# Optimization experiments

Hardware: AMD Instinct MI355X
Metric: run time of the kernel (lower is better)

Reference implementation:

```python
import jax, jax.numpy as jnp
import numpy as np


def setup_inputs() -> dict:
    key = jax.random.key(0)
    k_x, k_w = jax.random.split(key)
    S, B, D, H = 2048, 16, 1024, 1024
    X = jax.random.normal(k_x, (S, B, D), dtype=jnp.float32)
    hidden = jnp.zeros((B, H), dtype=jnp.float32)  # initial C_0
    W = jax.random.normal(k_w, (3 * H, D), dtype=jnp.float32) * 0.02
    b = jnp.zeros((3 * H,), dtype=jnp.float32)
    return {"X": X, "hidden": hidden, "W": W, "b": b}


def reference(X, hidden, W, b):
    # QRNNLayer forward, window=1, output_gate=True, zoneout off (eval).
    # Linear projection: [S,B,D] @ [D,3H] -> [S,B,3H]
    Y = jnp.einsum('sbd,hd->sbh', X, W) + b
    Z, F, O = jnp.split(Y, 3, axis=2)
    Z = jnp.tanh(Z)
    F = jax.nn.sigmoid(F)
    O = jax.nn.sigmoid(O)

    # ForgetMult fo-pool: C_t = F_t * Z_t + (1 - F_t) * C_{t-1}
    def step(c, fz):
        f, z = fz
        c = f * z + (1.0 - f) * c
        return c, c

    _, C = jax.lax.scan(step, hidden, (F, Z))  # C: [S,B,H]
    H_out = O * C
    return H_out, C[-1:, :, :]  # (H, last cell state [1,B,H])
```

## Files before the change

### kernel.cpp

```cpp
#include <hip/hip_runtime.h>
#include <hip/hip_bf16.h>
#include <cstdint>
#include <cstddef>

#define S_LEN 2048
#define BATCH 16
#define DIM   1024
#define HID   1024
#define M_TOT (S_LEN * BATCH)
#define N_TOT (3 * HID)
#define K_TOT DIM
#define NCHUNK 32
#define CHLEN (S_LEN / NCHUNK)

#define BM 256
#define BN 256
#define BK 32
#define NT (K_TOT / BK)
#define GRID_M (M_TOT / BM)
#define GRID_N (N_TOT / BN)
#define NWG (GRID_M * GRID_N)

typedef __bf16 bf16x8 __attribute__((ext_vector_type(8)));
typedef float  f32x4  __attribute__((ext_vector_type(4)));

__device__ __forceinline__ unsigned short f2bf(float f) {
    unsigned int u = __float_as_uint(f);
    u += 0x7FFFu + ((u >> 16) & 1u);
    return (unsigned short)(u >> 16);
}
__device__ __forceinline__ float bf2f(unsigned int s) {
    return __uint_as_float(s << 16);
}
__device__ __forceinline__ float fast_sigmoid(float x) { return 1.0f / (1.0f + __expf(-x)); }
__device__ __forceinline__ float fast_tanh(float x)    { return 2.0f / (1.0f + __expf(-2.0f * x)) - 1.0f; }

__global__ void __launch_bounds__(256) cvt_f32_bf16(const float* __restrict__ in,
                                                    unsigned short* __restrict__ out, int n4) {
    int i = blockIdx.x * blockDim.x + threadIdx.x;
    const int stride = gridDim.x * blockDim.x;
    for (; i < n4; i += stride) {
        const float4 v = reinterpret_cast<const float4*>(in)[i];
        ushort4 o;
        o.x = f2bf(v.x); o.y = f2bf(v.y); o.z = f2bf(v.z); o.w = f2bf(v.w);
        reinterpret_cast<ushort4*>(out)[i] = o;
    }
}

#define GLOAD_LDS16(gp, lp)                                                         \
    __builtin_amdgcn_global_load_lds((__attribute__((address_space(1))) void*)(gp), \
                                     (__attribute__((address_space(3))) void*)(lp), 16, 0, 0)

__global__ void __launch_bounds__(512, 2)
gemm_gates(const unsigned short* __restrict__ Xb,
           const unsigned short* __restrict__ Wb,
           const float* __restrict__ bias,
           unsigned short* __restrict__ gates) {
    __shared__ unsigned short As[4][BM * BK];
    __shared__ unsigned short Bs[4][BN * BK];

    const int tid  = threadIdx.x;
    const int lane = tid & 63;
    const int wid  = tid >> 6;
    const int wm   = wid >> 2;
    const int wn   = wid & 3;
    const int lr   = lane & 15;
    const int lc   = lane >> 4;

    const int swz = (blockIdx.x & 7) * (NWG / 8) + (blockIdx.x >> 3);
    const int bn = swz % GRID_N;
    const int bm = swz / GRID_N;

    const int srow  = tid >> 2;
    const int scolE = (((tid & 3) ^ ((tid >> 3) & 3)) << 3);
    const unsigned short* gA = Xb + (size_t)(bm * BM + srow) * K_TOT + scolE;
    const unsigned short* gB = Wb + (size_t)(bn * BN + srow) * K_TOT + scolE;
    unsigned short* lA = &As[0][tid * 8];
    unsigned short* lB = &Bs[0][tid * 8];

#define STAGE(tt) do {                                                   \
        const int _s = (tt) & 3; const int _k = (tt) * BK;               \
        GLOAD_LDS16(gA + _k,                lA + _s * (BM * BK));        \
        GLOAD_LDS16(gA + 128 * K_TOT + _k,  lA + _s * (BM * BK) + 4096); \
        GLOAD_LDS16(gB + _k,                lB + _s * (BN * BK));        \
        GLOAD_LDS16(gB + 128 * K_TOT + _k,  lB + _s * (BN * BK) + 4096); \
    } while (0)

    f32x4 acc[8][4];
#pragma unroll
    for (int m = 0; m < 8; ++m)
#pragma unroll
        for (int n = 0; n < 4; ++n) acc[m][n] = {0.0f, 0.0f, 0.0f, 0.0f};

    STAGE(0); STAGE(1); STAGE(2);
    asm volatile("s_waitcnt vmcnt(8)" ::: "memory");
    __builtin_amdgcn_s_barrier();

    for (int t = 0; t < NT; ++t) {
        const int s = t & 3;
        bf16x8 av[8], bv[4];
#pragma unroll
        for (int m = 0; m < 8; ++m) {
            const int row = wm * 128 + m * 16 + lr;
            av[m] = *reinterpret_cast<const bf16x8*>(
                &As[s][row * BK + ((lc ^ ((row >> 1) & 3)) << 3)]);
        }
#pragma unroll
        for (int n = 0; n < 4; ++n) {
            const int row = wn * 64 + n * 16 + lr;
            bv[n] = *reinterpret_cast<const bf16x8*>(
                &Bs[s][row * BK + ((lc ^ ((row >> 1) & 3)) << 3)]);
        }
        if (t + 3 < NT) {
            STAGE(t + 3);
            asm volatile("s_waitcnt vmcnt(8)" ::: "memory");
        } else if (t + 3 == NT) {
            asm volatile("s_waitcnt vmcnt(4)" ::: "memory");
        } else if (t + 2 == NT) {
            asm volatile("s_waitcnt vmcnt(0)" ::: "memory");
        }
        __builtin_amdgcn_s_barrier();
        __builtin_amdgcn_s_setprio(1);
#pragma unroll
        for (int m = 0; m < 8; ++m)
#pragma unroll
            for (int n = 0; n < 4; ++n)
                acc[m][n] = __builtin_amdgcn_mfma_f32_16x16x32_bf16(av[m], bv[n], acc[m][n], 0, 0, 0);
        __builtin_amdgcn_s_setprio(0);
        __builtin_amdgcn_s_barrier();
    }
#undef STAGE

    const int gate_id = bn >> 2;
    const int c0 = bn * BN + wn * 64 + lr;
    const int r0 = bm * BM + wm * 128 + ((lane >> 4) << 2);
#pragma unroll
    for (int n = 0; n < 4; ++n) {
        const int col = c0 + n * 16;
        const float bb = bias[col];
#pragma unroll
        for (int m = 0; m < 8; ++m) {
            const int rowb = r0 + m * 16;
#pragma unroll
            for (int r = 0; r < 4; ++r) {
                const float y = acc[m][n][r] + bb;
                const float g = (gate_id == 0) ? fast_tanh(y) : fast_sigmoid(y);
                gates[(size_t)(rowb + r) * N_TOT + col] = f2bf(g);
            }
        }
    }
}

__global__ void __launch_bounds__(256) scan_phase1(const unsigned short* __restrict__ gates,
                                                   float* __restrict__ Aprod,
                                                   float* __restrict__ Cend) {
    const int t = blockIdx.x * 256 + threadIdx.x;
    const int hp = t & 511;
    const int b  = (t >> 9) & (BATCH - 1);
    const int chunk = t >> 13;
    float c0 = 0.f, c1 = 0.f, a0 = 1.f, a1 = 1.f;
    const int m0 = chunk * (CHLEN * BATCH) + b;
    const unsigned short* gz = gates + (size_t)m0 * N_TOT + hp * 2;
#pragma unroll 4
    for (int i = 0; i < CHLEN; ++i) {
        const unsigned short* p = gz + (size_t)i * BATCH * N_TOT;
        const unsigned int zz = *reinterpret_cast<const unsigned int*>(p);
        const unsigned int ff = *reinterpret_cast<const unsigned int*>(p + HID);
        const float z0 = bf2f(zz & 0xffffu), z1 = bf2f(zz >> 16);
        const float f0 = bf2f(ff & 0xffffu), f1 = bf2f(ff >> 16);
        const float o0 = 1.f - f0, o1 = 1.f - f1;
        c0 = f0 * z0 + o0 * c0;  c1 = f1 * z1 + o1 * c1;
        a0 *= o0;                a1 *= o1;
    }
    const int idx = chunk * (BATCH * HID) + b * HID + hp * 2;
    *reinterpret_cast<float2*>(&Aprod[idx]) = make_float2(a0, a1);
    *reinterpret_cast<float2*>(&Cend[idx])  = make_float2(c0, c1);
}

__global__ void __launch_bounds__(256) scan_combine(const float* __restrict__ Aprod,
                                                    const float* __restrict__ Cend,
                                                    const float* __restrict__ hidden,
                                                    float* __restrict__ Cstart,
                                                    float* __restrict__ c_last) {
    const int t = blockIdx.x * 256 + threadIdx.x;
    float c = hidden[t];
#pragma unroll
    for (int j = 0; j < NCHUNK; ++j) {
        const int idx = j * (BATCH * HID) + t;
        Cstart[idx] = c;
        c = Aprod[idx] * c + Cend[idx];
    }
    c_last[t] = c;
}

__global__ void __launch_bounds__(256) scan_phase3(const unsigned short* __restrict__ gates,
                                                   const float* __restrict__ Cstart,
                                                   float* __restrict__ Hout) {
    const int t = blockIdx.x * 256 + threadIdx.x;
    const int hp = t & 511;
    const int b  = (t >> 9) & (BATCH - 1);
    const int chunk = t >> 13;
    const int idx = chunk * (BATCH * HID) + b * HID + hp * 2;
    float2 cs = *reinterpret_cast<const float2*>(&Cstart[idx]);
    float c0 = cs.x, c1 = cs.y;
    const int m0 = chunk * (CHLEN * BATCH) + b;
    const unsigned short* gz = gates + (size_t)m0 * N_TOT + hp * 2;
#pragma unroll 4
    for (int i = 0; i < CHLEN; ++i) {
        const unsigned short* p = gz + (size_t)i * BATCH * N_TOT;
        const unsigned int zz = *reinterpret_cast<const unsigned int*>(p);
        const unsigned int ff = *reinterpret_cast<const unsigned int*>(p + HID);
        const unsigned int oo = *reinterpret_cast<const unsigned int*>(p + 2 * HID);
        const float z0 = bf2f(zz & 0xffffu), z1 = bf2f(zz >> 16);
        const float f0 = bf2f(ff & 0xffffu), f1 = bf2f(ff >> 16);
        const float g0 = bf2f(oo & 0xffffu), g1 = bf2f(oo >> 16);
        c0 = f0 * z0 + (1.f - f0) * c0;
        c1 = f1 * z1 + (1.f - f1) * c1;
        const int m = m0 + i * BATCH;
        *reinterpret_cast<float2*>(&Hout[(size_t)m * HID + hp * 2]) = make_float2(g0 * c0, g1 * c1);
    }
}

extern "C" void kernel_launch(void* const* d_in, const int* in_sizes, int n_in,
                              void* d_out, int out_size, void* d_ws, size_t ws_size,
                              hipStream_t stream) {
    const float* X      = (const float*)d_in[0];
    const float* hidden = (const float*)d_in[1];
    const float* W      = (const float*)d_in[2];
    const float* bias   = (const float*)d_in[3];
    float* out    = (float*)d_out;
    float* c_last = out + (size_t)M_TOT * HID;

    char* ws = (char*)d_ws;
    unsigned short* Xb    = (unsigned short*)ws;
    unsigned short* Wb    = (unsigned short*)(ws + (size_t)M_TOT * K_TOT * 2);
    unsigned short* gates = Wb + (size_t)N_TOT * K_TOT;
    float* Aprod  = (float*)(gates + (size_t)M_TOT * N_TOT);
    float* Cend   = Aprod + (size_t)NCHUNK * BATCH * HID;
    float* Cstart = Cend  + (size_t)NCHUNK * BATCH * HID;

    cvt_f32_bf16<<<dim3(2048), dim3(256), 0, stream>>>(X, Xb, (int)(M_TOT * K_TOT / 4));
    cvt_f32_bf16<<<dim3(512),  dim3(256), 0, stream>>>(W, Wb, (int)(N_TOT * K_TOT / 4));
    gemm_gates<<<dim3(NWG), dim3(512), 0, stream>>>(Xb, Wb, bias, gates);
    scan_phase1<<<dim3(1024), dim3(256), 0, stream>>>(gates, Aprod, Cend);
    scan_combine<<<dim3(64), dim3(256), 0, stream>>>(Aprod, Cend, hidden, Cstart, c_last);
    scan_phase3<<<dim3(1024), dim3(256), 0, stream>>>(gates, Cstart, out);
}
```

Baseline: 442.2 us.

## Switch GEMM to 32x32x16 MFMA with four-phase interleaved LDS loads and prefetch

Replaces the 16x16x32 bf16 MFMA tiling with 32x32x16 MFMAs, using fewer and larger accumulator tiles per wave. Each K-step is split into four phases, each loading part of the A/B fragments from LDS, issuing one quarter of the next stage's global-to-LDS copies, and running a group of MFMAs. The goal is to cut LDS fragment reads per FLOP and to overlap LDS reads and global prefetch with matrix math. In exchange it adds more barriers per iteration and changes the epilogue's output row mapping, which must match the 32x32 accumulator layout.

```diff
diff --git a/kernel.cpp b/kernel.cpp
--- a/kernel.cpp
+++ b/kernel.cpp
@@ -22,7 +22,7 @@
 #define NWG (GRID_M * GRID_N)
 
 typedef __bf16 bf16x8 __attribute__((ext_vector_type(8)));
-typedef float  f32x4  __attribute__((ext_vector_type(4)));
+typedef float  f32x16 __attribute__((ext_vector_type(16)));
 
 __device__ __forceinline__ unsigned short f2bf(float f) {
     unsigned int u = __float_as_uint(f);
@@ -64,8 +64,8 @@
     const int wid  = tid >> 6;
     const int wm   = wid >> 2;
     const int wn   = wid & 3;
-    const int lr   = lane & 15;
-    const int lc   = lane >> 4;
+    const int l31  = lane & 31;
+    const int lhi  = lane >> 5;
 
     const int swz = (blockIdx.x & 7) * (NWG / 8) + (blockIdx.x >> 3);
     const int bn = swz % GRID_N;
@@ -78,41 +78,85 @@
     unsigned short* lA = &As[0][tid * 8];
     unsigned short* lB = &Bs[0][tid * 8];
 
-#define STAGE(tt) do {                                                   \
-        const int _s = (tt) & 3; const int _k = (tt) * BK;               \
-        GLOAD_LDS16(gA + _k,                lA + _s * (BM * BK));        \
-        GLOAD_LDS16(gA + 128 * K_TOT + _k,  lA + _s * (BM * BK) + 4096); \
-        GLOAD_LDS16(gB + _k,                lB + _s * (BN * BK));        \
-        GLOAD_LDS16(gB + 128 * K_TOT + _k,  lB + _s * (BN * BK) + 4096); \
+#define STAGE_I(tt, i) do { const int _s = (tt) & 3;                                             \
+        if ((i) < 2) GLOAD_LDS16(gA + (size_t)(i) * 128 * K_TOT + (tt) * BK,                     \
+                                 lA + _s * (BM * BK) + (i) * 4096);                              \
+        else         GLOAD_LDS16(gB + (size_t)((i) - 2) * 128 * K_TOT + (tt) * BK,               \
+                                 lB + _s * (BN * BK) + ((i) - 2) * 4096);                        \
     } while (0)
 
-    f32x4 acc[8][4];
-#pragma unroll
-    for (int m = 0; m < 8; ++m)
-#pragma unroll
-        for (int n = 0; n < 4; ++n) acc[m][n] = {0.0f, 0.0f, 0.0f, 0.0f};
-
-    STAGE(0); STAGE(1); STAGE(2);
+#define LDA_F(dst, s, m, kk) do {                                               \
+        const int _r  = wm * 128 + (m) * 32 + l31;                              \
+        const int _pg = ((kk) * 2 + lhi) ^ ((_r >> 1) & 3);                     \
+        dst = *reinterpret_cast<const bf16x8*>(&As[s][_r * BK + _pg * 8]); } while (0)
+#define LDB_F(dst, s, n, kk) do {                                               \
+        const int _r  = wn * 64 + (n) * 32 + l31;                               \
+        const int _pg = ((kk) * 2 + lhi) ^ ((_r >> 1) & 3);                     \
+        dst = *reinterpret_cast<const bf16x8*>(&Bs[s][_r * BK + _pg * 8]); } while (0)
+
+    f32x16 acc[4][2];
+#pragma unroll
+    for (int m = 0; m < 4; ++m)
+#pragma unroll
+        for (int n = 0; n < 2; ++n)
+#pragma unroll
+            for (int r = 0; r < 16; ++r) acc[m][n][r] = 0.0f;
+
+    bf16x8 a[4][2], b[2][2];
+
+    STAGE_I(0, 0); STAGE_I(0, 1); STAGE_I(0, 2); STAGE_I(0, 3);
+    STAGE_I(1, 0); STAGE_I(1, 1); STAGE_I(1, 2); STAGE_I(1, 3);
+    STAGE_I(2, 0); STAGE_I(2, 1); STAGE_I(2, 2); STAGE_I(2, 3);
     asm volatile("s_waitcnt vmcnt(8)" ::: "memory");
     __builtin_amdgcn_s_barrier();
 
+#pragma unroll 1
     for (int t = 0; t < NT; ++t) {
         const int s = t & 3;
-        bf16x8 av[8], bv[4];
-#pragma unroll
-        for (int m = 0; m < 8; ++m) {
-            const int row = wm * 128 + m * 16 + lr;
-            av[m] = *reinterpret_cast<const bf16x8*>(
-                &As[s][row * BK + ((lc ^ ((row >> 1) & 3)) << 3)]);
-        }
-#pragma unroll
-        for (int n = 0; n < 4; ++n) {
-            const int row = wn * 64 + n * 16 + lr;
-            bv[n] = *reinterpret_cast<const bf16x8*>(
-                &Bs[s][row * BK + ((lc ^ ((row >> 1) & 3)) << 3)]);
-        }
+#pragma unroll
+        for (int mi = 0; mi < 2; ++mi)
+#pragma unroll
+            for (int kk = 0; kk < 2; ++kk) LDA_F(a[mi][kk], s, mi, kk);
+#pragma unroll
+        for (int kk = 0; kk < 2; ++kk) LDB_F(b[0][kk], s, 0, kk);
+        if (t + 3 < NT) STAGE_I(t + 3, 0);
+        __builtin_amdgcn_s_barrier();
+        __builtin_amdgcn_s_setprio(1);
+#pragma unroll
+        for (int mi = 0; mi < 2; ++mi)
+#pragma unroll
+            for (int kk = 0; kk < 2; ++kk)
+                acc[mi][0] = __builtin_amdgcn_mfma_f32_32x32x16_bf16(a[mi][kk], b[0][kk], acc[mi][0], 0, 0, 0);
+        __builtin_amdgcn_s_setprio(0);
+        __builtin_amdgcn_s_barrier();
+#pragma unroll
+        for (int mi = 0; mi < 2; ++mi)
+#pragma unroll
+            for (int kk = 0; kk < 2; ++kk) LDA_F(a[2 + mi][kk], s, 2 + mi, kk);
+        if (t + 3 < NT) STAGE_I(t + 3, 1);
+        __builtin_amdgcn_s_barrier();
+        __builtin_amdgcn_s_setprio(1);
+#pragma unroll
+        for (int mi = 0; mi < 2; ++mi)
+#pragma unroll
+            for (int kk = 0; kk < 2; ++kk)
+                acc[2 + mi][0] = __builtin_amdgcn_mfma_f32_32x32x16_bf16(a[2 + mi][kk], b[0][kk], acc[2 + mi][0], 0, 0, 0);
+        __builtin_amdgcn_s_setprio(0);
+        __builtin_amdgcn_s_barrier();
+#pragma unroll
+        for (int kk = 0; kk < 2; ++kk) LDB_F(b[1][kk], s, 1, kk);
+        if (t + 3 < NT) STAGE_I(t + 3, 2);
+        __builtin_amdgcn_s_barrier();
+        __builtin_amdgcn_s_setprio(1);
+#pragma unroll
+        for (int mi = 0; mi < 2; ++mi)
+#pragma unroll
+            for (int kk = 0; kk < 2; ++kk)
+                acc[mi][1] = __builtin_amdgcn_mfma_f32_32x32x16_bf16(a[mi][kk], b[1][kk], acc[mi][1], 0, 0, 0);
+        __builtin_amdgcn_s_setprio(0);
+        __builtin_amdgcn_s_barrier();
         if (t + 3 < NT) {
-            STAGE(t + 3);
+            STAGE_I(t + 3, 3);
             asm volatile("s_waitcnt vmcnt(8)" ::: "memory");
         } else if (t + 3 == NT) {
             asm volatile("s_waitcnt vmcnt(4)" ::: "memory");
@@ -122,30 +166,31 @@
         __builtin_amdgcn_s_barrier();
         __builtin_amdgcn_s_setprio(1);
 #pragma unroll
-        for (int m = 0; m < 8; ++m)
-#pragma unroll
-            for (int n = 0; n < 4; ++n)
-                acc[m][n] = __builtin_amdgcn_mfma_f32_16x16x32_bf16(av[m], bv[n], acc[m][n], 0, 0, 0);
-        __builtin_amdgcn_s_setprio(0);
-        __builtin_amdgcn_s_barrier();
-    }
-#undef STAGE
+        for (int mi = 0; mi < 2; ++mi)
+#pragma unroll
+            for (int kk = 0; kk < 2; ++kk)
+                acc[2 + mi][1] = __builtin_amdgcn_mfma_f32_32x32x16_bf16(a[2 + mi][kk], b[1][kk], acc[2 + mi][1], 0, 0, 0);
+        __builtin_amdgcn_s_setprio(0);
+        __builtin_amdgcn_s_barrier();
+    }
+#undef STAGE_I
+#undef LDA_F
+#undef LDB_F
 
     const int gate_id = bn >> 2;
-    const int c0 = bn * BN + wn * 64 + lr;
-    const int r0 = bm * BM + wm * 128 + ((lane >> 4) << 2);
-#pragma unroll
-    for (int n = 0; n < 4; ++n) {
-        const int col = c0 + n * 16;
+#pragma unroll
+    for (int n = 0; n < 2; ++n) {
+        const int col = bn * BN + wn * 64 + n * 32 + l31;
         const float bb = bias[col];
 #pragma unroll
-        for (int m = 0; m < 8; ++m) {
-            const int rowb = r0 + m * 16;
-#pragma unroll
-            for (int r = 0; r < 4; ++r) {
+        for (int m = 0; m < 4; ++m) {
+            const int rb = bm * BM + wm * 128 + m * 32 + 4 * lhi;
+#pragma unroll
+            for (int r = 0; r < 16; ++r) {
+                const int row = rb + (r & 3) + 8 * (r >> 2);
                 const float y = acc[m][n][r] + bb;
                 const float g = (gate_id == 0) ? fast_tanh(y) : fast_sigmoid(y);
-                gates[(size_t)(rowb + r) * N_TOT + col] = f2bf(g);
+                gates[(size_t)row * N_TOT + col] = f2bf(g);
             }
         }
     }
```

After: 476.0 us. 1.08x slower.

## Restructure GEMM main loop into 8-phase interleaved schedule with BK=64 double buffering

Applied to the files above, without the earlier changes.

Raises the K tile from 32 to 64 and switches from a 4-stage to a 2-stage LDS ring. The K loop is split into eight sub-phases per two tiles, so LDS fragment reads, global-to-LDS loads and MFMA quarter-blocks interleave with finer barriers. The LDS swizzle moves to an 8-way XOR to suit the wider rows. The aim is to hide load latency and LDS reads behind matrix-core work. The cost is many more barriers and a tight vmcnt accounting that is easy to get wrong.

```diff
diff --git a/kernel.cpp b/kernel.cpp
--- a/kernel.cpp
+++ b/kernel.cpp
@@ -15,8 +15,9 @@
 
 #define BM 256
 #define BN 256
-#define BK 32
+#define BK 64
 #define NT (K_TOT / BK)
+#define NITER (NT / 2)
 #define GRID_M (M_TOT / BM)
 #define GRID_N (N_TOT / BN)
 #define NWG (GRID_M * GRID_N)
@@ -56,8 +57,8 @@
            const unsigned short* __restrict__ Wb,
            const float* __restrict__ bias,
            unsigned short* __restrict__ gates) {
-    __shared__ unsigned short As[4][BM * BK];
-    __shared__ unsigned short Bs[4][BN * BK];
+    __shared__ unsigned short As[2][BM * BK];
+    __shared__ unsigned short Bs[2][BN * BK];
 
     const int tid  = threadIdx.x;
     const int lane = tid & 63;
@@ -65,26 +66,46 @@
     const int wm   = wid >> 2;
     const int wn   = wid & 3;
     const int lr   = lane & 15;
-    const int lc   = lane >> 4;
+    const int lc   = (lane >> 4) & 3;
 
     const int swz = (blockIdx.x & 7) * (NWG / 8) + (blockIdx.x >> 3);
     const int bn = swz % GRID_N;
     const int bm = swz / GRID_N;
 
-    const int srow  = tid >> 2;
-    const int scolE = (((tid & 3) ^ ((tid >> 3) & 3)) << 3);
-    const unsigned short* gA = Xb + (size_t)(bm * BM + srow) * K_TOT + scolE;
-    const unsigned short* gB = Wb + (size_t)(bn * BN + srow) * K_TOT + scolE;
-    unsigned short* lA = &As[0][tid * 8];
-    unsigned short* lB = &Bs[0][tid * 8];
-
-#define STAGE(tt) do {                                                   \
-        const int _s = (tt) & 3; const int _k = (tt) * BK;               \
-        GLOAD_LDS16(gA + _k,                lA + _s * (BM * BK));        \
-        GLOAD_LDS16(gA + 128 * K_TOT + _k,  lA + _s * (BM * BK) + 4096); \
-        GLOAD_LDS16(gB + _k,                lB + _s * (BN * BK));        \
-        GLOAD_LDS16(gB + 128 * K_TOT + _k,  lB + _s * (BN * BK) + 4096); \
-    } while (0)
+    const int srow  = tid >> 3;
+    const int scolE = (((tid & 7) ^ ((tid >> 3) & 7)) << 3);
+    const unsigned short* gAs = Xb + (size_t)(bm * BM + srow) * K_TOT + scolE;
+    const unsigned short* gBs = Wb + (size_t)(bn * BN + srow) * K_TOT + scolE;
+
+#define STAGE_A(T, q) GLOAD_LDS16(gAs + (size_t)(q) * 64 * K_TOT + (T) * BK, \
+                                  &As[(T) & 1][(q) * 4096 + tid * 8])
+#define STAGE_B(T, q) GLOAD_LDS16(gBs + (size_t)(q) * 64 * K_TOT + (T) * BK, \
+                                  &Bs[(T) & 1][(q) * 4096 + tid * 8])
+
+#define LDA(dst, s, mf, kw) do { const int _r = wm * 128 + (mf) * 16 + lr;            \
+        dst = *reinterpret_cast<const bf16x8*>(                                        \
+            &As[s][_r * 64 + (((((kw) << 2) | lc) ^ (_r & 7)) << 3)]); } while (0)
+#define LDB(dst, s, nf, kw) do { const int _r = wn * 64 + (nf) * 16 + lr;             \
+        dst = *reinterpret_cast<const bf16x8*>(                                        \
+            &Bs[s][_r * 64 + (((((kw) << 2) | lc) ^ (_r & 7)) << 3)]); } while (0)
+
+#define RD_A(s, MH) do { _Pragma("unroll") for (int mi = 0; mi < 4; ++mi) {           \
+        LDA(a[mi][0], s, (MH) * 4 + mi, 0); LDA(a[mi][1], s, (MH) * 4 + mi, 1); } } while (0)
+#define RD_B(dst, s, NH) do { _Pragma("unroll") for (int ni = 0; ni < 2; ++ni) {      \
+        LDB(dst[ni][0], s, (NH) * 2 + ni, 0); LDB(dst[ni][1], s, (NH) * 2 + ni, 1); } } while (0)
+
+#define MM16(A_, B_, M0, N0) do {                                                     \
+    _Pragma("unroll") for (int mi = 0; mi < 4; ++mi)                                  \
+    _Pragma("unroll") for (int ni = 0; ni < 2; ++ni) {                                \
+        acc[(M0) + mi][(N0) + ni] = __builtin_amdgcn_mfma_f32_16x16x32_bf16(          \
+            A_[mi][0], B_[ni][0], acc[(M0) + mi][(N0) + ni], 0, 0, 0);                \
+        acc[(M0) + mi][(N0) + ni] = __builtin_amdgcn_mfma_f32_16x16x32_bf16(          \
+            A_[mi][1], B_[ni][1], acc[(M0) + mi][(N0) + ni], 0, 0, 0);                \
+    } } while (0)
+
+#define BAR __builtin_amdgcn_s_barrier()
+#define SP1 __builtin_amdgcn_s_setprio(1)
+#define SP0 __builtin_amdgcn_s_setprio(0)
 
     f32x4 acc[8][4];
 #pragma unroll
@@ -92,58 +113,73 @@
 #pragma unroll
         for (int n = 0; n < 4; ++n) acc[m][n] = {0.0f, 0.0f, 0.0f, 0.0f};
 
-    STAGE(0); STAGE(1); STAGE(2);
-    asm volatile("s_waitcnt vmcnt(8)" ::: "memory");
-    __builtin_amdgcn_s_barrier();
-
-    for (int t = 0; t < NT; ++t) {
-        const int s = t & 3;
-        bf16x8 av[8], bv[4];
-#pragma unroll
-        for (int m = 0; m < 8; ++m) {
-            const int row = wm * 128 + m * 16 + lr;
-            av[m] = *reinterpret_cast<const bf16x8*>(
-                &As[s][row * BK + ((lc ^ ((row >> 1) & 3)) << 3)]);
-        }
-#pragma unroll
-        for (int n = 0; n < 4; ++n) {
-            const int row = wn * 64 + n * 16 + lr;
-            bv[n] = *reinterpret_cast<const bf16x8*>(
-                &Bs[s][row * BK + ((lc ^ ((row >> 1) & 3)) << 3)]);
-        }
-        if (t + 3 < NT) {
-            STAGE(t + 3);
-            asm volatile("s_waitcnt vmcnt(8)" ::: "memory");
-        } else if (t + 3 == NT) {
-            asm volatile("s_waitcnt vmcnt(4)" ::: "memory");
-        } else if (t + 2 == NT) {
-            asm volatile("s_waitcnt vmcnt(0)" ::: "memory");
-        }
-        __builtin_amdgcn_s_barrier();
-        __builtin_amdgcn_s_setprio(1);
-#pragma unroll
-        for (int m = 0; m < 8; ++m)
-#pragma unroll
-            for (int n = 0; n < 4; ++n)
-                acc[m][n] = __builtin_amdgcn_mfma_f32_16x16x32_bf16(av[m], bv[n], acc[m][n], 0, 0, 0);
-        __builtin_amdgcn_s_setprio(0);
-        __builtin_amdgcn_s_barrier();
-    }
-#undef STAGE
+    bf16x8 a[4][2], b[2][2], b2[2][2];
+
+    STAGE_A(0, 0); STAGE_A(0, 1); STAGE_A(0, 2); STAGE_A(0, 3);
+    STAGE_B(0, 0); STAGE_B(0, 1); STAGE_B(0, 2); STAGE_B(0, 3);
+    STAGE_A(1, 0); STAGE_A(1, 2);
+    STAGE_B(1, 0); STAGE_B(1, 1);
+    STAGE_A(1, 1); STAGE_A(1, 3);
+    asm volatile("s_waitcnt vmcnt(6)" ::: "memory");
+    BAR;
+
+#pragma unroll 1
+    for (int j = 0; j < NITER; ++j) {
+        const int t0 = 2 * j;
+        const int t1 = 2 * j + 1;
+        const bool st = (j < NITER - 1);
+        RD_A(0, 0); RD_B(b, 0, 0);
+        STAGE_B(t1, 2); STAGE_B(t1, 3);
+        BAR; SP1; MM16(a, b, 0, 0); SP0; BAR;
+        RD_B(b2, 0, 1);
+        if (st) { STAGE_A(t0 + 2, 0); STAGE_A(t0 + 2, 2); }
+        BAR; SP1; MM16(a, b2, 0, 2); SP0; BAR;
+        RD_A(0, 1);
+        if (st) { STAGE_B(t0 + 2, 0); STAGE_B(t0 + 2, 1); }
+        BAR; SP1; MM16(a, b, 4, 0); SP0; BAR;
+        if (st) { STAGE_A(t0 + 2, 1); STAGE_A(t0 + 2, 3); }
+        BAR; SP1; MM16(a, b2, 4, 2); SP0;
+        if (st) asm volatile("s_waitcnt vmcnt(6)" ::: "memory");
+        else    asm volatile("s_waitcnt vmcnt(0)" ::: "memory");
+        BAR;
+        RD_A(1, 0); RD_B(b, 1, 0);
+        if (st) { STAGE_B(t0 + 2, 2); STAGE_B(t0 + 2, 3); }
+        BAR; SP1; MM16(a, b, 0, 0); SP0; BAR;
+        RD_B(b2, 1, 1);
+        if (st) { STAGE_A(t1 + 2, 0); STAGE_A(t1 + 2, 2); }
+        BAR; SP1; MM16(a, b2, 0, 2); SP0; BAR;
+        RD_A(1, 1);
+        if (st) { STAGE_B(t1 + 2, 0); STAGE_B(t1 + 2, 1); }
+        BAR; SP1; MM16(a, b, 4, 0); SP0; BAR;
+        if (st) { STAGE_A(t1 + 2, 1); STAGE_A(t1 + 2, 3); }
+        BAR; SP1; MM16(a, b2, 4, 2); SP0;
+        if (st) asm volatile("s_waitcnt vmcnt(6)" ::: "memory");
+        BAR;
+    }
+#undef STAGE_A
+#undef STAGE_B
+#undef LDA
+#undef LDB
+#undef RD_A
+#undef RD_B
+#undef MM16
+#undef BAR
+#undef SP1
+#undef SP0
 
     const int gate_id = bn >> 2;
     const int c0 = bn * BN + wn * 64 + lr;
     const int r0 = bm * BM + wm * 128 + ((lane >> 4) << 2);
 #pragma unroll
-    for (int n = 0; n < 4; ++n) {
-        const int col = c0 + n * 16;
+    for (int nf = 0; nf < 4; ++nf) {
+        const int col = c0 + nf * 16;
         const float bb = bias[col];
 #pragma unroll
-        for (int m = 0; m < 8; ++m) {
-            const int rowb = r0 + m * 16;
+        for (int mf = 0; mf < 8; ++mf) {
+            const int rowb = r0 + mf * 16;
 #pragma unroll
             for (int r = 0; r < 4; ++r) {
-                const float y = acc[m][n][r] + bb;
+                const float y = acc[mf][nf][r] + bb;
                 const float g = (gate_id == 0) ? fast_tanh(y) : fast_sigmoid(y);
                 gates[(size_t)(rowb + r) * N_TOT + col] = f2bf(g);
             }
```

New measurement: 422.6 us. 1.05x faster.

## Stage GEMM epilogue through LDS, double-buffer K tiles, fuse bf16 conversions

Applied to the files above, without the earlier changes.

Merges the two fp32-to-bf16 conversion launches into one kernel. In the GEMM, the 4-stage LDS ring becomes 2-stage double buffering, which halves LDS use to 64KB so two blocks can fit per CU. The gate epilogue now writes tiles into swizzled LDS and stores them as 16-byte coalesced rows, replacing the scattered 2-byte global stores. The cost is less prefetch depth to hide latency and extra barriers in the epilogue.

```diff
diff --git a/kernel.cpp b/kernel.cpp
--- a/kernel.cpp
+++ b/kernel.cpp
@@ -35,15 +35,24 @@
 __device__ __forceinline__ float fast_sigmoid(float x) { return 1.0f / (1.0f + __expf(-x)); }
 __device__ __forceinline__ float fast_tanh(float x)    { return 2.0f / (1.0f + __expf(-2.0f * x)) - 1.0f; }
 
-__global__ void __launch_bounds__(256) cvt_f32_bf16(const float* __restrict__ in,
-                                                    unsigned short* __restrict__ out, int n4) {
-    int i = blockIdx.x * blockDim.x + threadIdx.x;
-    const int stride = gridDim.x * blockDim.x;
-    for (; i < n4; i += stride) {
-        const float4 v = reinterpret_cast<const float4*>(in)[i];
-        ushort4 o;
-        o.x = f2bf(v.x); o.y = f2bf(v.y); o.z = f2bf(v.z); o.w = f2bf(v.w);
-        reinterpret_cast<ushort4*>(out)[i] = o;
+__global__ void __launch_bounds__(256) cvt_both(const float* __restrict__ X,
+                                                const float* __restrict__ W,
+                                                unsigned short* __restrict__ Xb,
+                                                unsigned short* __restrict__ Wb) {
+    const int nx = (M_TOT * K_TOT) / 4;
+    const int nw = (N_TOT * K_TOT) / 4;
+    if (blockIdx.x < 2048) {
+        for (int i = blockIdx.x * 256 + threadIdx.x; i < nx; i += 2048 * 256) {
+            const float4 v = reinterpret_cast<const float4*>(X)[i];
+            ushort4 o; o.x = f2bf(v.x); o.y = f2bf(v.y); o.z = f2bf(v.z); o.w = f2bf(v.w);
+            reinterpret_cast<ushort4*>(Xb)[i] = o;
+        }
+    } else {
+        for (int i = (blockIdx.x - 2048) * 256 + threadIdx.x; i < nw; i += 512 * 256) {
+            const float4 v = reinterpret_cast<const float4*>(W)[i];
+            ushort4 o; o.x = f2bf(v.x); o.y = f2bf(v.y); o.z = f2bf(v.z); o.w = f2bf(v.w);
+            reinterpret_cast<ushort4*>(Wb)[i] = o;
+        }
     }
 }
 
@@ -56,8 +65,9 @@
            const unsigned short* __restrict__ Wb,
            const float* __restrict__ bias,
            unsigned short* __restrict__ gates) {
-    __shared__ unsigned short As[4][BM * BK];
-    __shared__ unsigned short Bs[4][BN * BK];
+    __shared__ __align__(16) unsigned short LDSbuf[4 * BM * BK];
+#define AS(s) (LDSbuf + (s) * (BM * BK))
+#define BS(s) (LDSbuf + 2 * (BM * BK) + (s) * (BN * BK))
 
     const int tid  = threadIdx.x;
     const int lane = tid & 63;
@@ -75,15 +85,12 @@
     const int scolE = (((tid & 3) ^ ((tid >> 3) & 3)) << 3);
     const unsigned short* gA = Xb + (size_t)(bm * BM + srow) * K_TOT + scolE;
     const unsigned short* gB = Wb + (size_t)(bn * BN + srow) * K_TOT + scolE;
-    unsigned short* lA = &As[0][tid * 8];
-    unsigned short* lB = &Bs[0][tid * 8];
-
-#define STAGE(tt) do {                                                   \
-        const int _s = (tt) & 3; const int _k = (tt) * BK;               \
-        GLOAD_LDS16(gA + _k,                lA + _s * (BM * BK));        \
-        GLOAD_LDS16(gA + 128 * K_TOT + _k,  lA + _s * (BM * BK) + 4096); \
-        GLOAD_LDS16(gB + _k,                lB + _s * (BN * BK));        \
-        GLOAD_LDS16(gB + 128 * K_TOT + _k,  lB + _s * (BN * BK) + 4096); \
+
+#define STAGE_T(tt) do { const int _s = (tt) & 1; const int _k = (tt) * BK;          \
+        GLOAD_LDS16(gA + _k,                 AS(_s) + tid * 8);                      \
+        GLOAD_LDS16(gA + 128 * K_TOT + _k,   AS(_s) + 4096 + tid * 8);               \
+        GLOAD_LDS16(gB + _k,                 BS(_s) + tid * 8);                      \
+        GLOAD_LDS16(gB + 128 * K_TOT + _k,   BS(_s) + 4096 + tid * 8);               \
     } while (0)
 
     f32x4 acc[8][4];
@@ -92,34 +99,30 @@
 #pragma unroll
         for (int n = 0; n < 4; ++n) acc[m][n] = {0.0f, 0.0f, 0.0f, 0.0f};
 
-    STAGE(0); STAGE(1); STAGE(2);
-    asm volatile("s_waitcnt vmcnt(8)" ::: "memory");
+    STAGE_T(0); STAGE_T(1);
+    asm volatile("s_waitcnt vmcnt(4)" ::: "memory");
     __builtin_amdgcn_s_barrier();
 
+#pragma unroll 2
     for (int t = 0; t < NT; ++t) {
-        const int s = t & 3;
+        const int s = t & 1;
         bf16x8 av[8], bv[4];
 #pragma unroll
         for (int m = 0; m < 8; ++m) {
             const int row = wm * 128 + m * 16 + lr;
             av[m] = *reinterpret_cast<const bf16x8*>(
-                &As[s][row * BK + ((lc ^ ((row >> 1) & 3)) << 3)]);
+                &AS(s)[row * BK + ((lc ^ ((row >> 1) & 3)) << 3)]);
         }
 #pragma unroll
         for (int n = 0; n < 4; ++n) {
             const int row = wn * 64 + n * 16 + lr;
             bv[n] = *reinterpret_cast<const bf16x8*>(
-                &Bs[s][row * BK + ((lc ^ ((row >> 1) & 3)) << 3)]);
-        }
-        if (t + 3 < NT) {
-            STAGE(t + 3);
-            asm volatile("s_waitcnt vmcnt(8)" ::: "memory");
-        } else if (t + 3 == NT) {
-            asm volatile("s_waitcnt vmcnt(4)" ::: "memory");
-        } else if (t + 2 == NT) {
-            asm volatile("s_waitcnt vmcnt(0)" ::: "memory");
-        }
+                &BS(s)[row * BK + ((lc ^ ((row >> 1) & 3)) << 3)]);
+        }
+        asm volatile("s_waitcnt lgkmcnt(0)" ::: "memory");
+        __builtin_amdgcn_sched_barrier(0);
         __builtin_amdgcn_s_barrier();
+        if (t + 2 < NT) STAGE_T(t + 2);
         __builtin_amdgcn_s_setprio(1);
 #pragma unroll
         for (int m = 0; m < 8; ++m)
@@ -127,28 +130,59 @@
             for (int n = 0; n < 4; ++n)
                 acc[m][n] = __builtin_amdgcn_mfma_f32_16x16x32_bf16(av[m], bv[n], acc[m][n], 0, 0, 0);
         __builtin_amdgcn_s_setprio(0);
+        if (t + 2 < NT) {
+            asm volatile("s_waitcnt vmcnt(4)" ::: "memory");
+        } else if (t + 1 < NT) {
+            asm volatile("s_waitcnt vmcnt(0)" ::: "memory");
+        }
         __builtin_amdgcn_s_barrier();
     }
-#undef STAGE
+#undef STAGE_T
 
     const int gate_id = bn >> 2;
-    const int c0 = bn * BN + wn * 64 + lr;
-    const int r0 = bm * BM + wm * 128 + ((lane >> 4) << 2);
-#pragma unroll
-    for (int n = 0; n < 4; ++n) {
-        const int col = c0 + n * 16;
-        const float bb = bias[col];
-#pragma unroll
-        for (int m = 0; m < 8; ++m) {
-            const int rowb = r0 + m * 16;
-#pragma unroll
-            for (int r = 0; r < 4; ++r) {
-                const float y = acc[m][n][r] + bb;
-                const float g = (gate_id == 0) ? fast_tanh(y) : fast_sigmoid(y);
-                gates[(size_t)(rowb + r) * N_TOT + col] = f2bf(g);
+    const int gr   = lane & 31;
+    const int rsub = lane >> 5;
+#pragma unroll
+    for (int p = 0; p < 2; ++p) {
+        if (wm == p) {
+            const int rl0 = (lane >> 4) << 2;
+            const int cl0 = wn * 64 + lr;
+#pragma unroll
+            for (int nf = 0; nf < 4; ++nf) {
+                const int col = cl0 + nf * 16;
+                const float bb = bias[bn * BN + col];
+#pragma unroll
+                for (int mf = 0; mf < 8; ++mf) {
+#pragma unroll
+                    for (int r = 0; r < 4; ++r) {
+                        const int row = rl0 + mf * 16 + r;
+                        const float y = acc[mf][nf][r] + bb;
+                        const float g = (gate_id == 0) ? fast_tanh(y) : fast_sigmoid(y);
+                        const int phys = (col >> 3) ^ (row & 7);
+                        LDSbuf[row * 256 + (phys << 3) + (col & 7)] = f2bf(g);
+                    }
+                }
             }
         }
-    }
+        asm volatile("s_waitcnt lgkmcnt(0)" ::: "memory");
+        __builtin_amdgcn_sched_barrier(0);
+        __builtin_amdgcn_s_barrier();
+#pragma unroll
+        for (int i = 0; i < 8; ++i) {
+            const int rl = wid * 16 + i * 2 + rsub;
+            const int phys = gr ^ (rl & 7);
+            const bf16x8 v = *reinterpret_cast<const bf16x8*>(&LDSbuf[rl * 256 + (phys << 3)]);
+            *reinterpret_cast<bf16x8*>(
+                &gates[(size_t)(bm * BM + p * 128 + rl) * N_TOT + bn * BN + gr * 8]) = v;
+        }
+        if (p == 0) {
+            asm volatile("s_waitcnt lgkmcnt(0)" ::: "memory");
+            __builtin_amdgcn_sched_barrier(0);
+            __builtin_amdgcn_s_barrier();
+        }
+    }
+#undef AS
+#undef BS
 }
 
 __global__ void __launch_bounds__(256) scan_phase1(const unsigned short* __restrict__ gates,
@@ -239,8 +273,7 @@
     float* Cend   = Aprod + (size_t)NCHUNK * BATCH * HID;
     float* Cstart = Cend  + (size_t)NCHUNK * BATCH * HID;
 
-    cvt_f32_bf16<<<dim3(2048), dim3(256), 0, stream>>>(X, Xb, (int)(M_TOT * K_TOT / 4));
-    cvt_f32_bf16<<<dim3(512),  dim3(256), 0, stream>>>(W, Wb, (int)(N_TOT * K_TOT / 4));
+    cvt_both<<<dim3(2560), dim3(256), 0, stream>>>(X, W, Xb, Wb);
     gemm_gates<<<dim3(NWG), dim3(512), 0, stream>>>(Xb, Wb, bias, gates);
     scan_phase1<<<dim3(1024), dim3(256), 0, stream>>>(gates, Aprod, Cend);
     scan_combine<<<dim3(64), dim3(256), 0, stream>>>(Aprod, Cend, hidden, Cstart, c_last);
```

Result: no change. 446.8 us (+1.0%).
